# Kernel tuning notes

Measured on AMD Instinct MI355X. Metric: run time of the kernel, lower is better.

## Reference

```python
import jax, jax.numpy as jnp
import numpy as np

D_MODEL = 1024
NUM_HEADS = 16
HEAD_DIM = D_MODEL // NUM_HEADS
SCALE = 1.0 / np.sqrt(HEAD_DIM).astype(np.float32)


def setup_inputs() -> dict:
    key = jax.random.key(0)
    k1, k2, k3, k4 = jax.random.split(key, 4)
    B, L = 1, 4096
    s = 0.02
    x = jax.random.normal(k1, (B, L, D_MODEL), dtype=jnp.float32)
    W_qkv = jax.random.normal(k2, (D_MODEL, 3 * D_MODEL), dtype=jnp.float32) * s
    W_o = jax.random.normal(k3, (D_MODEL, D_MODEL), dtype=jnp.float32) * s
    b_o = jax.random.normal(k4, (D_MODEL,), dtype=jnp.float32) * s
    return {"x": x, "W_qkv": W_qkv, "W_o": W_o, "b_o": b_o}


def reference(x, W_qkv, W_o, b_o):
    B, L, D = x.shape
    H, Hd = NUM_HEADS, HEAD_DIM
    qkv = x @ W_qkv                          # [B, L, 3D]
    qkv = qkv.reshape(B, L, 3, H, Hd)
    q = jnp.transpose(qkv[:, :, 0], (0, 2, 1, 3))  # [B, H, L, Hd]
    k = jnp.transpose(qkv[:, :, 1], (0, 2, 1, 3))
    v = jnp.transpose(qkv[:, :, 2], (0, 2, 1, 3))
    scores = jnp.einsum("bhqd,bhkd->bhqk", q, k) * SCALE  # [B, H, L, L]
    attn = jax.nn.softmax(scores, axis=-1)
    out = jnp.einsum("bhqk,bhkd->bhqd", attn, v)          # [B, H, L, Hd]
    out = jnp.transpose(out, (0, 2, 1, 3)).reshape(B, L, D)
    return out @ W_o + b_o
```

## Files before the change

### kernel.cpp

```cpp
#include <hip/hip_runtime.h>
#include <stdint.h>


#define L_SEQ 4096
#define DM 1024
#define NHEAD 16
#define HDIM 64
#define ATT_SCALE 0.125f
#define LOG2E 1.4426950408889634f
#define CSC (ATT_SCALE * LOG2E)

typedef __attribute__((ext_vector_type(8))) __bf16 bf16x8;
typedef __attribute__((ext_vector_type(4))) __bf16 bf16x4;
typedef __attribute__((ext_vector_type(4))) float f32x4;
typedef __attribute__((ext_vector_type(8))) float f32x8;
typedef __attribute__((ext_vector_type(4))) short short4v;
typedef __attribute__((ext_vector_type(8))) short short8v;

#define GLL16(g, l) __builtin_amdgcn_global_load_lds( \
    (__attribute__((address_space(1))) void*)(g),     \
    (__attribute__((address_space(3))) void*)(l), 16, 0, 0)

#define MFMA32(a, b, c) __builtin_amdgcn_mfma_f32_16x16x32_bf16((a), (b), (c), 0, 0, 0)

__device__ __forceinline__ short f2bf(float f) {
  uint32_t u = __builtin_bit_cast(uint32_t, f);
  u += 0x7fffu + ((u >> 16) & 1u);
  return (short)(u >> 16);
}

__global__ __launch_bounds__(256)
void prep_kernel(const float* __restrict__ x, short* __restrict__ xb,
                 const float* __restrict__ Wq, short* __restrict__ wqt,
                 const float* __restrict__ Wo, short* __restrict__ wot) {
  __shared__ __align__(16) short tbuf[64 * 66];
  const int tid = threadIdx.x;
  const int blk = blockIdx.x;
  if (blk < 4096) {
    int i = blk * 256 + tid;
    float4 v = ((const float4*)x)[i];
    short4 o;
    o.x = f2bf(v.x); o.y = f2bf(v.y); o.z = f2bf(v.z); o.w = f2bf(v.w);
    ((short4*)xb)[i] = o;
    return;
  }
  const float* W; short* Wt; int N, nb, kb;
  const int K = 1024;
  if (blk < 4096 + 768) {
    int b = blk - 4096;
    W = Wq; Wt = wqt; N = 3072; nb = (b % 48) * 64; kb = (b / 48) * 64;
  } else {
    int b = blk - (4096 + 768);
    W = Wo; Wt = wot; N = 1024; nb = (b % 16) * 64; kb = (b / 16) * 64;
  }
#pragma unroll
  for (int i = 0; i < 16; i++) {
    int idx = tid + i * 256;
    int r = idx >> 6, c = idx & 63;
    tbuf[r * 66 + c] = f2bf(W[(size_t)(kb + r) * N + nb + c]);
  }
  __syncthreads();
#pragma unroll
  for (int i = 0; i < 16; i++) {
    int idx = tid + i * 256;
    int r = idx >> 6, c = idx & 63;
    Wt[(size_t)(nb + r) * K + kb + c] = tbuf[c * 66 + r];
  }
}

__global__ __launch_bounds__(256, 3)
void gemm_qkv(const short* __restrict__ A, const short* __restrict__ Bt,
              short* __restrict__ qkv, short* __restrict__ vtout, int K) {
  __shared__ __align__(16) short smem[24576];
  const int tid = threadIdx.x;
  const int lane = tid & 63;
  const int wave = tid >> 6;
  const int quad = lane >> 4;
  const int cl = lane & 15;
  const int m0 = blockIdx.x * 128;
  const int n0 = blockIdx.y * 128;
  const int wm = (wave >> 1) * 64;
  const int wn = (wave & 1) * 64;

  f32x4 acc[4][4] = {};

  const short* ap[2]; const short* bp[2]; int lo[2];
#pragma unroll
  for (int i = 0; i < 2; i++) {
    int ci = i * 256 + tid;
    int row = ci & 127, c = ci >> 7;
    ap[i] = A + (size_t)(m0 + row) * K + c * 8;
    bp[i] = Bt + (size_t)(n0 + row) * K + c * 8;
    lo[i] = ci * 8;
  }
  short* pA0 = smem;          short* pA1 = smem + 4096;   short* pA2 = smem + 8192;
  short* pB0 = smem + 12288;  short* pB1 = smem + 16384;  short* pB2 = smem + 20480;
#define QST(kt, Ab, Bb)                              \
  {                                                  \
    _Pragma("unroll")                                \
    for (int i = 0; i < 2; i++) {                    \
      GLL16(ap[i] + (kt) * 32, (Ab) + lo[i]);        \
      GLL16(bp[i] + (kt) * 32, (Bb) + lo[i]);        \
    }                                                \
  }
#define QCOMP(Ab, Bb)                                                          \
  {                                                                            \
    bf16x8 af[4], bfr[4];                                                      \
    _Pragma("unroll")                                                          \
    for (int t4 = 0; t4 < 4; t4++) {                                           \
      af[t4]  = *(const bf16x8*)((Ab) + (quad * 128 + wm + t4 * 16 + cl) * 8); \
      bfr[t4] = *(const bf16x8*)((Bb) + (quad * 128 + wn + t4 * 16 + cl) * 8); \
    }                                                                          \
    _Pragma("unroll")                                                          \
    for (int mt = 0; mt < 4; mt++)                                             \
      _Pragma("unroll")                                                        \
      for (int nt = 0; nt < 4; nt++)                                           \
        acc[mt][nt] = MFMA32(af[mt], bfr[nt], acc[mt][nt]);                    \
  }

  const int NT = K >> 5;
  QST(0, pA0, pB0);
  QST(1, pA1, pB1);
  for (int t = 0; t < NT - 1; t++) {
    asm volatile("s_waitcnt vmcnt(4)" ::: "memory");
    __builtin_amdgcn_s_barrier();
    __builtin_amdgcn_sched_barrier(0);
    if (t + 2 < NT) QST(t + 2, pA2, pB2);
    QCOMP(pA0, pB0);
    short* tA = pA0; pA0 = pA1; pA1 = pA2; pA2 = tA;
    short* tB = pB0; pB0 = pB1; pB1 = pB2; pB2 = tB;
  }
  asm volatile("s_waitcnt vmcnt(0)" ::: "memory");
  __builtin_amdgcn_s_barrier();
  __builtin_amdgcn_sched_barrier(0);
  QCOMP(pA0, pB0);
#undef QST
#undef QCOMP

  const int which = n0 >> 10;
  if (which == 2) {
#pragma unroll
    for (int mt = 0; mt < 4; mt++)
#pragma unroll
      for (int nt = 0; nt < 4; nt++) {
        int col = n0 + wn + nt * 16 + cl;
        int hd = col & 63;
        int hidx = (col >> 6) & 15;
        int row0 = m0 + wm + mt * 16 + quad * 4;
        short4v pk;
#pragma unroll
        for (int r = 0; r < 4; r++) pk[r] = f2bf(acc[mt][nt][r]);
        *(short4v*)(vtout + ((size_t)hidx * HDIM + hd) * L_SEQ + row0) = pk;
      }
  } else {
    const float sc = (which == 0) ? CSC : 1.0f;
    short* Ct = smem;
#pragma unroll
    for (int p = 0; p < 2; p++) {
      __syncthreads();
      if ((wave & 1) == p) {
#pragma unroll
        for (int mt = 0; mt < 4; mt++)
#pragma unroll
          for (int nt = 0; nt < 4; nt++) {
            int m = wm + mt * 16 + quad * 4;
            int c = nt * 16 + cl;
#pragma unroll
            for (int r = 0; r < 4; r++)
              Ct[(m + r) * 72 + c] = f2bf(acc[mt][nt][r] * sc);
          }
      }
      __syncthreads();
      int hidx = ((n0 + p * 64) >> 6) & 15;
      size_t base = ((size_t)which * NHEAD + hidx) * L_SEQ * HDIM;
      int m = tid >> 1;
      int j0 = (tid & 1) * 4;
#pragma unroll
      for (int i = 0; i < 4; i++) {
        short8v v = *(const short8v*)(Ct + m * 72 + (j0 + i) * 8);
        *(short8v*)(qkv + base + (size_t)(m0 + m) * HDIM + (j0 + i) * 8) = v;
      }
    }
  }
}

__global__ __launch_bounds__(256, 2)
void gemm_out(const short* __restrict__ A, const short* __restrict__ Bt,
              float* __restrict__ C, const float* __restrict__ bias, int K) {
  __shared__ __align__(16) short smem[18432];
  const int tid = threadIdx.x;
  const int lane = tid & 63;
  const int wave = tid >> 6;
  const int quad = lane >> 4;
  const int cl = lane & 15;
  const int m0 = blockIdx.x * 128;
  const int n0 = blockIdx.y * 64;
  const int wm = (wave >> 1) * 64;
  const int wn = (wave & 1) * 32;
  const int N = 1024;

  f32x4 acc[4][2] = {};

  const short* ap[2]; const short* bp1; int loA[2], loB;
#pragma unroll
  for (int i = 0; i < 2; i++) {
    int ci = i * 256 + tid;
    ap[i] = A + (size_t)(m0 + (ci & 127)) * K + (ci >> 7) * 8;
    loA[i] = ci * 8;
  }
  bp1 = Bt + (size_t)(n0 + (tid & 63)) * K + (tid >> 6) * 8;
  loB = tid * 8;
  short* pA0 = smem;          short* pA1 = smem + 4096;   short* pA2 = smem + 8192;
  short* pB0 = smem + 12288;  short* pB1 = smem + 14336;  short* pB2 = smem + 16384;
#define OST(kt, Ab, Bb)                              \
  {                                                  \
    _Pragma("unroll")                                \
    for (int i = 0; i < 2; i++)                      \
      GLL16(ap[i] + (kt) * 32, (Ab) + loA[i]);       \
    GLL16(bp1 + (kt) * 32, (Bb) + loB);              \
  }
#define OCOMP(Ab, Bb)                                                          \
  {                                                                            \
    bf16x8 af[4], bfr[2];                                                      \
    _Pragma("unroll")                                                          \
    for (int t4 = 0; t4 < 4; t4++)                                             \
      af[t4] = *(const bf16x8*)((Ab) + (quad * 128 + wm + t4 * 16 + cl) * 8);  \
    _Pragma("unroll")                                                          \
    for (int t4 = 0; t4 < 2; t4++)                                             \
      bfr[t4] = *(const bf16x8*)((Bb) + (quad * 64 + wn + t4 * 16 + cl) * 8);  \
    _Pragma("unroll")                                                          \
    for (int mt = 0; mt < 4; mt++)                                             \
      _Pragma("unroll")                                                        \
      for (int nt = 0; nt < 2; nt++)                                           \
        acc[mt][nt] = MFMA32(af[mt], bfr[nt], acc[mt][nt]);                    \
  }

  const int NT = K >> 5;
  OST(0, pA0, pB0);
  OST(1, pA1, pB1);
  for (int t = 0; t < NT - 1; t++) {
    asm volatile("s_waitcnt vmcnt(3)" ::: "memory");
    __builtin_amdgcn_s_barrier();
    __builtin_amdgcn_sched_barrier(0);
    if (t + 2 < NT) OST(t + 2, pA2, pB2);
    OCOMP(pA0, pB0);
    short* tA = pA0; pA0 = pA1; pA1 = pA2; pA2 = tA;
    short* tB = pB0; pB0 = pB1; pB1 = pB2; pB2 = tB;
  }
  asm volatile("s_waitcnt vmcnt(0)" ::: "memory");
  __builtin_amdgcn_s_barrier();
  __builtin_amdgcn_sched_barrier(0);
  OCOMP(pA0, pB0);
#undef OST
#undef OCOMP

#pragma unroll
  for (int mt = 0; mt < 4; mt++)
#pragma unroll
    for (int nt = 0; nt < 2; nt++) {
      int col = n0 + wn + nt * 16 + cl;
      float b = bias[col];
#pragma unroll
      for (int r = 0; r < 4; r++) {
        int row = m0 + wm + mt * 16 + quad * 4 + r;
        C[(size_t)row * N + col] = acc[mt][nt][r] + b;
      }
    }
}

#define KVB 128
__global__ __launch_bounds__(512, 4)
void attn_kernel(const short* __restrict__ qkv, const short* __restrict__ vt,
                 short* __restrict__ aout) {
  __shared__ __align__(16) short Ks[2][KVB * HDIM];
  __shared__ __align__(16) short Vs[2][HDIM * KVB];
  __shared__ float lbuf[512];
  const int tid = threadIdx.x, lane = tid & 63, wave = tid >> 6;
  const int quad = lane >> 4, cl = lane & 15;
  const int kg = wave & 1;
  const int qg = wave >> 1;
  const int bid = blockIdx.x;
  const int h  = ((bid & 7) << 1) | ((bid >> 3) & 1);
  const int qb = bid >> 4;
  const short* Qg = qkv + (size_t)h * L_SEQ * HDIM;
  const short* Kg = qkv + ((size_t)NHEAD + h) * L_SEQ * HDIM;
  const short* Vg = vt + (size_t)h * HDIM * L_SEQ;
  const int keyoff = ((cl >> 2) << 3) | (cl & 3);

  bf16x8 qf[2][2];
#pragma unroll
  for (int qs = 0; qs < 2; qs++) {
    int qrow = qb * 128 + qg * 32 + qs * 16 + cl;
    qf[qs][0] = *(const bf16x8*)(Qg + (size_t)qrow * HDIM + quad * 8);
    qf[qs][1] = *(const bf16x8*)(Qg + (size_t)qrow * HDIM + 32 + quad * 8);
  }
  const short8v ov = {0x3F80, 0x3F80, 0x3F80, 0x3F80, 0x3F80, 0x3F80, 0x3F80, 0x3F80};
  const bf16x8 ones = __builtin_bit_cast(bf16x8, ov);
  f32x4 o_l[2] = {};
  f32x4 o_acc[4][2] = {};

  int koff[2][2][2];
  int voff[2][4];
#pragma unroll
  for (int kslab = 0; kslab < 2; kslab++) {
#pragma unroll
    for (int b = 0; b < 2; b++) {
      int krow = kg * 64 + kslab * 32 + keyoff + b * 4;
      int sw = (krow & 3) | (((krow >> 3) & 1) << 2);
#pragma unroll
      for (int ks = 0; ks < 2; ks++)
        koff[kslab][b][ks] = (krow * 8 + ((ks * 4 + quad) ^ sw)) * 8;
    }
#pragma unroll
    for (int G = 0; G < 4; G++) {
      int vrow = G * 16 + cl;
      int sw = (vrow & 3) | (((vrow >> 3) & 1) << 2);
      voff[kslab][G] = (vrow * 16 + ((kg * 8 + kslab * 4 + quad) ^ sw)) * 8;
    }
  }

  const short* kp[2]; const short* vp[2]; int ldsoK[2], ldsoV[2];
#pragma unroll
  for (int i = 0; i < 2; i++) {
    int ciK = i * 512 + tid;
    int rowK = ciK >> 3;
    int swK = (rowK & 3) | (((rowK >> 3) & 1) << 2);
    int cK = (ciK & 7) ^ swK;
    kp[i] = Kg + (size_t)rowK * HDIM + cK * 8;
    ldsoK[i] = ciK * 8;
    int ciV = i * 512 + tid;
    int rowV = ciV >> 4;
    int swV = (rowV & 3) | (((rowV >> 3) & 1) << 2);
    int cV = (ciV & 15) ^ swV;
    vp[i] = Vg + (size_t)rowV * L_SEQ + cV * 8;
    ldsoV[i] = ciV * 8;
  }
#define STAGE(t, buf)                                        \
  {                                                          \
    _Pragma("unroll")                                        \
    for (int i = 0; i < 2; i++) {                            \
      GLL16(kp[i] + (t) * KVB * HDIM, &Ks[buf][ldsoK[i]]);   \
      GLL16(vp[i] + (t) * KVB, &Vs[buf][ldsoV[i]]);          \
    }                                                        \
  }

  STAGE(0, 0);
#pragma unroll 2
  for (int t = 0; t < L_SEQ / KVB; t++) {
    const int cur = t & 1;
    __syncthreads();
    if (t + 1 < L_SEQ / KVB) STAGE(t + 1, cur ^ 1);
    const short* Kb = Ks[cur];
    const short* Vb = Vs[cur];

#pragma unroll
    for (int kslab = 0; kslab < 2; kslab++) {
      f32x4 s[2][2] = {};
      __builtin_amdgcn_s_setprio(1);
#pragma unroll
      for (int b = 0; b < 2; b++)
#pragma unroll
        for (int ks = 0; ks < 2; ks++) {
          bf16x8 kf = *(const bf16x8*)(Kb + koff[kslab][b][ks]);
#pragma unroll
          for (int qs = 0; qs < 2; qs++)
            s[qs][b] = MFMA32(kf, qf[qs][ks], s[qs][b]);
        }
      __builtin_amdgcn_s_setprio(0);

      bf16x8 vfr[4];
#pragma unroll
      for (int G = 0; G < 4; G++)
        vfr[G] = *(const bf16x8*)(Vb + voff[kslab][G]);

      bf16x8 pb0;
      {
        f32x8 pv8;
#pragma unroll
        for (int b = 0; b < 2; b++)
#pragma unroll
          for (int r = 0; r < 4; r++)
            pv8[b * 4 + r] = __builtin_amdgcn_exp2f(s[0][b][r]);
        pb0 = __builtin_convertvector(pv8, bf16x8);
      }

      __builtin_amdgcn_s_setprio(1);
      o_l[0] = MFMA32(ones, pb0, o_l[0]);
#pragma unroll
      for (int G = 0; G < 4; G++)
        o_acc[G][0] = MFMA32(vfr[G], pb0, o_acc[G][0]);
      __builtin_amdgcn_s_setprio(0);

      bf16x8 pb1;
      {
        f32x8 pv8;
#pragma unroll
        for (int b = 0; b < 2; b++)
#pragma unroll
          for (int r = 0; r < 4; r++)
            pv8[b * 4 + r] = __builtin_amdgcn_exp2f(s[1][b][r]);
        pb1 = __builtin_convertvector(pv8, bf16x8);
      }

      __builtin_amdgcn_s_setprio(1);
      o_l[1] = MFMA32(ones, pb1, o_l[1]);
#pragma unroll
      for (int G = 0; G < 4; G++)
        o_acc[G][1] = MFMA32(vfr[G], pb1, o_acc[G][1]);
      __builtin_amdgcn_s_setprio(0);
    }
  }
#undef STAGE

  __syncthreads();
  float* ored = (float*)&Ks[0][0];
  if (kg == 1) {
#pragma unroll
    for (int G = 0; G < 4; G++)
#pragma unroll
      for (int qs = 0; qs < 2; qs++)
        *(f32x4*)&ored[(((qg * 4 + G) * 2 + qs) * 64 + lane) * 4] = o_acc[G][qs];
#pragma unroll
    for (int qs = 0; qs < 2; qs++)
      lbuf[(qg * 2 + qs) * 64 + lane] = o_l[qs][0];
  }
  __syncthreads();
  if (kg == 0) {
#pragma unroll
    for (int qs = 0; qs < 2; qs++) {
      float l = o_l[qs][0] + lbuf[(qg * 2 + qs) * 64 + lane];
      float inv = 1.f / l;
      int token = qb * 128 + qg * 32 + qs * 16 + cl;
#pragma unroll
      for (int G = 0; G < 4; G++) {
        f32x4 part = *(const f32x4*)&ored[(((qg * 4 + G) * 2 + qs) * 64 + lane) * 4];
        f32x4 sc = (o_acc[G][qs] + part) * inv;
        bf16x4 pk = __builtin_convertvector(sc, bf16x4);
        *(short4v*)(aout + (size_t)token * DM + h * HDIM + G * 16 + quad * 4) =
            __builtin_bit_cast(short4v, pk);
      }
    }
  }
}

extern "C" void kernel_launch(void* const* d_in, const int* in_sizes, int n_in,
                              void* d_out, int out_size, void* d_ws, size_t ws_size,
                              hipStream_t stream) {
  const float* x    = (const float*)d_in[0];
  const float* Wqkv = (const float*)d_in[1];
  const float* Wo   = (const float*)d_in[2];
  const float* bo   = (const float*)d_in[3];
  char* ws = (char*)d_ws;
  short* xb    = (short*)(ws);
  short* wqkvt = (short*)(ws + (size_t)8 * 1024 * 1024);
  short* wot   = (short*)(ws + (size_t)14 * 1024 * 1024);
  short* qkv   = (short*)(ws + (size_t)16 * 1024 * 1024);
  short* vt    = (short*)(ws + (size_t)40 * 1024 * 1024);
  short* aout  = xb;
  float* out = (float*)d_out;

  prep_kernel<<<4096 + 768 + 256, 256, 0, stream>>>(x, xb, Wqkv, wqkvt, Wo, wot);
  gemm_qkv<<<dim3(32, 24), 256, 0, stream>>>(xb, wqkvt, qkv, vt, DM);
  attn_kernel<<<dim3(512), 512, 0, stream>>>(qkv, vt, aout);
  gemm_out<<<dim3(32, 16), 256, 0, stream>>>(aout, wot, out, bo, DM);
}
```

Baseline: 231.8 us.

## Halve attention query tile, read V directly from global, double occupancy

```diff
diff --git a/kernel.cpp b/kernel.cpp
--- a/kernel.cpp
+++ b/kernel.cpp
@@ -269,12 +269,11 @@
 }
 
 #define KVB 128
-__global__ __launch_bounds__(512, 4)
+__global__ __launch_bounds__(512, 8)
 void attn_kernel(const short* __restrict__ qkv, const short* __restrict__ vt,
                  short* __restrict__ aout) {
   __shared__ __align__(16) short Ks[2][KVB * HDIM];
-  __shared__ __align__(16) short Vs[2][HDIM * KVB];
-  __shared__ float lbuf[512];
+  __shared__ float lbuf[256];
   const int tid = threadIdx.x, lane = tid & 63, wave = tid >> 6;
   const int quad = lane >> 4, cl = lane & 15;
   const int kg = wave & 1;
@@ -287,39 +286,32 @@
   const short* Vg = vt + (size_t)h * HDIM * L_SEQ;
   const int keyoff = ((cl >> 2) << 3) | (cl & 3);
 
-  bf16x8 qf[2][2];
-#pragma unroll
-  for (int qs = 0; qs < 2; qs++) {
-    int qrow = qb * 128 + qg * 32 + qs * 16 + cl;
-    qf[qs][0] = *(const bf16x8*)(Qg + (size_t)qrow * HDIM + quad * 8);
-    qf[qs][1] = *(const bf16x8*)(Qg + (size_t)qrow * HDIM + 32 + quad * 8);
+  bf16x8 qf[2];
+  {
+    int qrow = qb * 64 + qg * 16 + cl;
+    qf[0] = *(const bf16x8*)(Qg + (size_t)qrow * HDIM + quad * 8);
+    qf[1] = *(const bf16x8*)(Qg + (size_t)qrow * HDIM + 32 + quad * 8);
   }
   const short8v ov = {0x3F80, 0x3F80, 0x3F80, 0x3F80, 0x3F80, 0x3F80, 0x3F80, 0x3F80};
   const bf16x8 ones = __builtin_bit_cast(bf16x8, ov);
-  f32x4 o_l[2] = {};
-  f32x4 o_acc[4][2] = {};
-
-  int koff[2][2][2];
-  int voff[2][4];
-#pragma unroll
-  for (int kslab = 0; kslab < 2; kslab++) {
-#pragma unroll
-    for (int b = 0; b < 2; b++) {
-      int krow = kg * 64 + kslab * 32 + keyoff + b * 4;
-      int sw = (krow & 3) | (((krow >> 3) & 1) << 2);
-#pragma unroll
-      for (int ks = 0; ks < 2; ks++)
-        koff[kslab][b][ks] = (krow * 8 + ((ks * 4 + quad) ^ sw)) * 8;
-    }
-#pragma unroll
-    for (int G = 0; G < 4; G++) {
-      int vrow = G * 16 + cl;
-      int sw = (vrow & 3) | (((vrow >> 3) & 1) << 2);
-      voff[kslab][G] = (vrow * 16 + ((kg * 8 + kslab * 4 + quad) ^ sw)) * 8;
-    }
-  }
-
-  const short* kp[2]; const short* vp[2]; int ldsoK[2], ldsoV[2];
+  f32x4 o_l = {};
+  f32x4 o_acc[4] = {};
+
+  int koff2[2];
+  {
+    int krow = kg * 64 + keyoff;
+    int sw = (krow & 3) | (((krow >> 3) & 1) << 2);
+#pragma unroll
+    for (int ks = 0; ks < 2; ks++)
+      koff2[ks] = (krow * 8 + ((ks * 4 + quad) ^ sw)) * 8;
+  }
+  int vo[4];
+#pragma unroll
+  for (int G = 0; G < 4; G++)
+    vo[G] = (G * 16 + cl) * L_SEQ + quad * 8;
+  const int kg64 = kg * 64;
+
+  const short* kp[2]; int ldsoK[2];
 #pragma unroll
   for (int i = 0; i < 2; i++) {
     int ciK = i * 512 + tid;
@@ -328,20 +320,12 @@
     int cK = (ciK & 7) ^ swK;
     kp[i] = Kg + (size_t)rowK * HDIM + cK * 8;
     ldsoK[i] = ciK * 8;
-    int ciV = i * 512 + tid;
-    int rowV = ciV >> 4;
-    int swV = (rowV & 3) | (((rowV >> 3) & 1) << 2);
-    int cV = (ciV & 15) ^ swV;
-    vp[i] = Vg + (size_t)rowV * L_SEQ + cV * 8;
-    ldsoV[i] = ciV * 8;
   }
 #define STAGE(t, buf)                                        \
   {                                                          \
     _Pragma("unroll")                                        \
-    for (int i = 0; i < 2; i++) {                            \
+    for (int i = 0; i < 2; i++)                              \
       GLL16(kp[i] + (t) * KVB * HDIM, &Ks[buf][ldsoK[i]]);   \
-      GLL16(vp[i] + (t) * KVB, &Vs[buf][ldsoV[i]]);          \
-    }                                                        \
   }
 
   STAGE(0, 0);
@@ -351,62 +335,44 @@
     __syncthreads();
     if (t + 1 < L_SEQ / KVB) STAGE(t + 1, cur ^ 1);
     const short* Kb = Ks[cur];
-    const short* Vb = Vs[cur];
+    const int tkey = t * KVB + kg64;
 
 #pragma unroll
     for (int kslab = 0; kslab < 2; kslab++) {
-      f32x4 s[2][2] = {};
+      f32x4 s[2] = {};
       __builtin_amdgcn_s_setprio(1);
 #pragma unroll
       for (int b = 0; b < 2; b++)
 #pragma unroll
         for (int ks = 0; ks < 2; ks++) {
-          bf16x8 kf = *(const bf16x8*)(Kb + koff[kslab][b][ks]);
-#pragma unroll
-          for (int qs = 0; qs < 2; qs++)
-            s[qs][b] = MFMA32(kf, qf[qs][ks], s[qs][b]);
+          bf16x8 kf = *(const bf16x8*)(Kb + koff2[ks] + kslab * 2048 + b * 256);
+          s[b] = MFMA32(kf, qf[ks], s[b]);
         }
       __builtin_amdgcn_s_setprio(0);
 
-      bf16x8 vfr[4];
-#pragma unroll
-      for (int G = 0; G < 4; G++)
-        vfr[G] = *(const bf16x8*)(Vb + voff[kslab][G]);
-
-      bf16x8 pb0;
+      bf16x8 v0 = *(const bf16x8*)(Vg + vo[0] + tkey + kslab * 32);
+      bf16x8 v1 = *(const bf16x8*)(Vg + vo[1] + tkey + kslab * 32);
+
+      bf16x8 pb;
       {
         f32x8 pv8;
 #pragma unroll
         for (int b = 0; b < 2; b++)
 #pragma unroll
           for (int r = 0; r < 4; r++)
-            pv8[b * 4 + r] = __builtin_amdgcn_exp2f(s[0][b][r]);
-        pb0 = __builtin_convertvector(pv8, bf16x8);
+            pv8[b * 4 + r] = __builtin_amdgcn_exp2f(s[b][r]);
+        pb = __builtin_convertvector(pv8, bf16x8);
       }
 
+      bf16x8 v2 = *(const bf16x8*)(Vg + vo[2] + tkey + kslab * 32);
+      bf16x8 v3 = *(const bf16x8*)(Vg + vo[3] + tkey + kslab * 32);
+
       __builtin_amdgcn_s_setprio(1);
-      o_l[0] = MFMA32(ones, pb0, o_l[0]);
-#pragma unroll
-      for (int G = 0; G < 4; G++)
-        o_acc[G][0] = MFMA32(vfr[G], pb0, o_acc[G][0]);
-      __builtin_amdgcn_s_setprio(0);
-
-      bf16x8 pb1;
-      {
-        f32x8 pv8;
-#pragma unroll
-        for (int b = 0; b < 2; b++)
-#pragma unroll
-          for (int r = 0; r < 4; r++)
-            pv8[b * 4 + r] = __builtin_amdgcn_exp2f(s[1][b][r]);
-        pb1 = __builtin_convertvector(pv8, bf16x8);
-      }
-
-      __builtin_amdgcn_s_setprio(1);
-      o_l[1] = MFMA32(ones, pb1, o_l[1]);
-#pragma unroll
-      for (int G = 0; G < 4; G++)
-        o_acc[G][1] = MFMA32(vfr[G], pb1, o_acc[G][1]);
+      o_l = MFMA32(ones, pb, o_l);
+      o_acc[0] = MFMA32(v0, pb, o_acc[0]);
+      o_acc[1] = MFMA32(v1, pb, o_acc[1]);
+      o_acc[2] = MFMA32(v2, pb, o_acc[2]);
+      o_acc[3] = MFMA32(v3, pb, o_acc[3]);
       __builtin_amdgcn_s_setprio(0);
     }
   }
@@ -417,28 +383,21 @@
   if (kg == 1) {
 #pragma unroll
     for (int G = 0; G < 4; G++)
-#pragma unroll
-      for (int qs = 0; qs < 2; qs++)
-        *(f32x4*)&ored[(((qg * 4 + G) * 2 + qs) * 64 + lane) * 4] = o_acc[G][qs];
-#pragma unroll
-    for (int qs = 0; qs < 2; qs++)
-      lbuf[(qg * 2 + qs) * 64 + lane] = o_l[qs][0];
+      *(f32x4*)&ored[((qg * 4 + G) * 64 + lane) * 4] = o_acc[G];
+    lbuf[qg * 64 + lane] = o_l[0];
   }
   __syncthreads();
   if (kg == 0) {
-#pragma unroll
-    for (int qs = 0; qs < 2; qs++) {
-      float l = o_l[qs][0] + lbuf[(qg * 2 + qs) * 64 + lane];
-      float inv = 1.f / l;
-      int token = qb * 128 + qg * 32 + qs * 16 + cl;
-#pragma unroll
-      for (int G = 0; G < 4; G++) {
-        f32x4 part = *(const f32x4*)&ored[(((qg * 4 + G) * 2 + qs) * 64 + lane) * 4];
-        f32x4 sc = (o_acc[G][qs] + part) * inv;
-        bf16x4 pk = __builtin_convertvector(sc, bf16x4);
-        *(short4v*)(aout + (size_t)token * DM + h * HDIM + G * 16 + quad * 4) =
-            __builtin_bit_cast(short4v, pk);
-      }
+    float l = o_l[0] + lbuf[qg * 64 + lane];
+    float inv = 1.f / l;
+    int token = qb * 64 + qg * 16 + cl;
+#pragma unroll
+    for (int G = 0; G < 4; G++) {
+      f32x4 part = *(const f32x4*)&ored[((qg * 4 + G) * 64 + lane) * 4];
+      f32x4 sc = (o_acc[G] + part) * inv;
+      bf16x4 pk = __builtin_convertvector(sc, bf16x4);
+      *(short4v*)(aout + (size_t)token * DM + h * HDIM + G * 16 + quad * 4) =
+          __builtin_bit_cast(short4v, pk);
     }
   }
 }
@@ -461,6 +420,6 @@
 
   prep_kernel<<<4096 + 768 + 256, 256, 0, stream>>>(x, xb, Wqkv, wqkvt, Wo, wot);
   gemm_qkv<<<dim3(32, 24), 256, 0, stream>>>(xb, wqkvt, qkv, vt, DM);
-  attn_kernel<<<dim3(512), 512, 0, stream>>>(qkv, vt, aout);
+  attn_kernel<<<dim3(1024), 512, 0, stream>>>(qkv, vt, aout);
   gemm_out<<<dim3(32, 16), 256, 0, stream>>>(aout, wot, out, bo, DM);
 }
```

Result: slower. 524.3 us (+126.1%).
